# Kernel optimization log

Measured on AMD Instinct MI355X. Metric: run time of the kernel, lower is better.

Reference implementation:

```python
import jax, jax.numpy as jnp
import numpy as np

D_DEC = 256  # decoder_size; W columns are [decoder | encoder] per the torch concat order


def setup_inputs() -> dict:
    key = jax.random.key(0)
    k1, k2, k3, k4 = jax.random.split(key, 4)
    B, S, E, D, A = 32, 4096, 256, 256, 256
    decoder_hidden = jax.random.normal(k1, (1, B, D), dtype=jnp.float32)
    encoder_outputs = jax.random.normal(k2, (S, B, E), dtype=jnp.float32)
    W = jax.random.normal(k3, (A, D + E), dtype=jnp.float32) / np.sqrt(D + E)
    b = jax.random.normal(k4, (A,), dtype=jnp.float32) * 0.02
    return {"decoder_hidden": decoder_hidden, "encoder_outputs": encoder_outputs, "W": W, "b": b}


def reference(decoder_hidden, encoder_outputs, W, b):
    # decoder_hidden: [1,B,D] -> [B,D]; encoder_outputs: [S,B,E] -> [B,S,E]
    dh = decoder_hidden[0]
    eo = jnp.transpose(encoder_outputs, (1, 0, 2))
    # Split the concat-linear: cat([dec, enc]) @ W.T == dec @ Wd.T + enc @ We.T
    Wd, We = W[:, :D_DEC], W[:, D_DEC:]
    # scores: tanh(linear) summed over attn dim -> [B,S]
    proj = dh @ Wd.T + b  # [B,A]
    attn = jnp.tanh(proj[:, None, :] + jnp.einsum('bse,ae->bsa', eo, We))
    scores = jnp.sum(attn, axis=2)  # [B,S]
    attn_softmax = jax.nn.softmax(scores, axis=1)  # [B,S]
    attended = jnp.einsum('bs,bse->be', attn_softmax, eo)  # [B,E]
    encoder_norms = jnp.linalg.norm(eo, axis=2)  # [B,S]
    attn_map = attn_softmax * encoder_norms
    return attended, attn_map
```

## Files before the change

### kernel.cpp

```cpp
#include <hip/hip_runtime.h>
#include <math.h>

#define B_  32
#define S_  4096
#define E_  256
#define A_  256
#define DE_ 512
#define SCH 128

typedef __attribute__((ext_vector_type(8))) short short8;
typedef __attribute__((ext_vector_type(4))) float f32x4;

__device__ inline unsigned short f2bf(float x) {
    unsigned int u = __float_as_uint(x);
    u += 0x7FFFu + ((u >> 16) & 1u);
    return (unsigned short)(u >> 16);
}
__device__ inline float bf2f(unsigned short h) {
    return __uint_as_float(((unsigned int)h) << 16);
}
__device__ inline float tanh_fast(float x) {
    x = fminf(fmaxf(x, -15.f), 15.f);
    float t = __expf(2.f * x);
    return (t - 1.f) * __builtin_amdgcn_rcpf(t + 1.f);
}

__global__ __launch_bounds__(256) void wprep_kernel(
    const float* __restrict__ W, unsigned short* __restrict__ wepk)
{
    const int idx = blockIdx.x * 256 + threadIdx.x;
    const int c     = idx >> 11;
    const int r     = idx & 2047;
    const int plane = r >> 10;
    const int kg    = (r >> 8) & 3;
    const int a     = r & 255;
    const float* src = W + (size_t)a * DE_ + E_ + c * 32 + kg * 8;
    unsigned int pk[4];
    #pragma unroll
    for (int j = 0; j < 4; ++j) {
        float x0 = src[2 * j], x1 = src[2 * j + 1];
        unsigned int u0 = __float_as_uint(x0) & 0xFFFF0000u;
        unsigned int u1 = __float_as_uint(x1) & 0xFFFF0000u;
        if (plane) {
            unsigned short l0 = f2bf(x0 - __uint_as_float(u0));
            unsigned short l1 = f2bf(x1 - __uint_as_float(u1));
            pk[j] = (unsigned int)l0 | ((unsigned int)l1 << 16);
        } else {
            pk[j] = (u0 >> 16) | u1;
        }
    }
    *(uint4*)&wepk[(size_t)idx * 8] = make_uint4(pk[0], pk[1], pk[2], pk[3]);
}

__global__ __launch_bounds__(256) void proj_kernel(
    const float* __restrict__ dh, const float* __restrict__ W,
    const float* __restrict__ bias, float* __restrict__ proj)
{
    __shared__ float dh_lds[E_];
    const int b = blockIdx.x;
    const int a = threadIdx.x;
    dh_lds[a] = dh[b * E_ + a];
    __syncthreads();
    float acc = bias[a];
    const float* wrow = W + (size_t)a * DE_;
    #pragma unroll
    for (int d = 0; d < E_; d += 4) {
        float4 w = *(const float4*)(wrow + d);
        acc += dh_lds[d] * w.x + dh_lds[d+1] * w.y
             + dh_lds[d+2] * w.z + dh_lds[d+3] * w.w;
    }
    proj[b * A_ + a] = acc;
}

__global__ __launch_bounds__(256, 4) void scores_kernel(
    const float* __restrict__ eo,
    const unsigned short* __restrict__ wepk,
    const float* __restrict__ proj,
    float* __restrict__ scores, float* __restrict__ nsq)
{
    __shared__ __align__(16) unsigned short we_hl[2 * 4 * 256 * 8];
    __shared__ __align__(16) unsigned short eo_hl[2 * 4 * 64 * 8];

    const int tid = threadIdx.x;
    const int b   = blockIdx.x & (B_ - 1);
    const int s0  = (blockIdx.x / B_) * 64;
    const int w   = tid >> 6;
    const int l   = tid & 63;
    const int lq  = l >> 4;
    const int lr  = l & 15;
    const int lqx = (lq & 1) << 2;

    float pr[4];
    #pragma unroll
    for (int nt = 0; nt < 4; ++nt) pr[nt] = proj[b * A_ + w * 64 + nt * 16 + lr];

    f32x4 acc[4][4];
    #pragma unroll
    for (int i = 0; i < 4; ++i)
        #pragma unroll
        for (int j = 0; j < 4; ++j)
            acc[i][j] = (f32x4){0.f, 0.f, 0.f, 0.f};

    const int erow0 = tid >> 3;
    const int ekq   = tid & 7;
    const int ekg   = ekq >> 1, ehalf = ekq & 1;
    const int esw   = (ekg & 1) << 2;
    float nacc[2] = {0.f, 0.f};

    for (int kc = 0, c = 0; kc < E_; kc += 32, ++c) {
        __syncthreads();
        #pragma unroll
        for (int it = 0; it < 2; ++it) {
            const int row = it * 32 + erow0;
            float4 v = *(const float4*)(eo + (size_t)(s0 + row) * (B_ * E_)
                                           + b * E_ + kc + ekq * 4);
            nacc[it] += v.x*v.x + v.y*v.y + v.z*v.z + v.w*v.w;
            unsigned int ux = __float_as_uint(v.x) & 0xFFFF0000u;
            unsigned int uy = __float_as_uint(v.y) & 0xFFFF0000u;
            unsigned int uz = __float_as_uint(v.z) & 0xFFFF0000u;
            unsigned int uw = __float_as_uint(v.w) & 0xFFFF0000u;
            unsigned int hp0 = (ux >> 16) | uy;
            unsigned int hp1 = (uz >> 16) | uw;
            unsigned int lp0 = (unsigned int)f2bf(v.x - __uint_as_float(ux))
                             | ((unsigned int)f2bf(v.y - __uint_as_float(uy)) << 16);
            unsigned int lp1 = (unsigned int)f2bf(v.z - __uint_as_float(uz))
                             | ((unsigned int)f2bf(v.w - __uint_as_float(uw)) << 16);
            const int u = ekg * 64 + (row ^ esw);
            *(uint2*)&eo_hl[(size_t)u * 8 + ehalf * 4]         = make_uint2(hp0, hp1);
            *(uint2*)&eo_hl[(size_t)(256 + u) * 8 + ehalf * 4] = make_uint2(lp0, lp1);
        }
        const unsigned short* gsrc = wepk + (size_t)c * 2048 * 8;
        #pragma unroll
        for (int it = 0; it < 8; ++it) {
            const int u = it * 256 + tid;
            __builtin_amdgcn_global_load_lds(
                (const __attribute__((address_space(1))) void*)(gsrc + (size_t)u * 8),
                (__attribute__((address_space(3))) void*)&we_hl[(size_t)u * 8],
                16, 0, 0);
        }
        __syncthreads();
        short8 bh[4], bl[4];
        #pragma unroll
        for (int nt = 0; nt < 4; ++nt) {
            int bunit = lq * 256 + w * 64 + nt * 16 + lr;
            bh[nt] = *(const short8*)&we_hl[(size_t)bunit * 8];
            bl[nt] = *(const short8*)&we_hl[(size_t)(1024 + bunit) * 8];
        }
        #pragma unroll
        for (int mt = 0; mt < 4; ++mt) {
            int aunit = lq * 64 + ((mt * 16 + lr) ^ lqx);
            short8 ah = *(const short8*)&eo_hl[(size_t)aunit * 8];
            short8 al = *(const short8*)&eo_hl[(size_t)(256 + aunit) * 8];
            #pragma unroll
            for (int nt = 0; nt < 4; ++nt) {
                acc[mt][nt] = __builtin_amdgcn_mfma_f32_16x16x32_bf16(ah, bh[nt], acc[mt][nt], 0, 0, 0);
                acc[mt][nt] = __builtin_amdgcn_mfma_f32_16x16x32_bf16(ah, bl[nt], acc[mt][nt], 0, 0, 0);
                acc[mt][nt] = __builtin_amdgcn_mfma_f32_16x16x32_bf16(al, bh[nt], acc[mt][nt], 0, 0, 0);
            }
        }
    }
    __syncthreads();

    float* red4  = (float*)we_hl;
    float* npart = red4 + 64 * 65;
    float* qpart = npart + 512;
    #pragma unroll
    for (int mt = 0; mt < 4; ++mt) {
        #pragma unroll
        for (int r = 0; r < 4; ++r) {
            float s = 0.f;
            #pragma unroll
            for (int nt = 0; nt < 4; ++nt)
                s += tanh_fast(pr[nt] + acc[mt][nt][r]);
            red4[(w * 16 + lr) * 65 + (mt * 16 + lq * 4 + r)] = s;
        }
    }
    npart[tid]       = nacc[0];
    npart[256 + tid] = nacc[1];
    __syncthreads();
    {
        const int r = tid & 63, q = tid >> 6;
        float s = 0.f;
        #pragma unroll
        for (int c2 = q * 16; c2 < q * 16 + 16; ++c2) s += red4[c2 * 65 + r];
        qpart[q * 64 + r] = s;
    }
    __syncthreads();
    if (tid < 64) {
        scores[b * S_ + s0 + tid] = qpart[tid] + qpart[64 + tid]
                                  + qpart[128 + tid] + qpart[192 + tid];
        const int base = (tid >> 5) * 256 + (tid & 31) * 8;
        float nq = 0.f;
        #pragma unroll
        for (int q2 = 0; q2 < 8; ++q2) nq += npart[base + q2];
        nsq[b * S_ + s0 + tid] = nq;
    }
}

__global__ __launch_bounds__(256) void softmax_kernel(
    float* __restrict__ nsq_p, float* __restrict__ out)
{
    __shared__ float red[256];
    const int b = blockIdx.x;
    const int tid = threadIdx.x;
    float* scores = out + B_ * E_;

    float v[16];
    float m = -1e30f;
    #pragma unroll
    for (int i = 0; i < 16; ++i) {
        v[i] = scores[b * S_ + i * 256 + tid];
        m = fmaxf(m, v[i]);
    }
    red[tid] = m;
    __syncthreads();
    for (int off = 128; off > 0; off >>= 1) {
        if (tid < off) red[tid] = fmaxf(red[tid], red[tid + off]);
        __syncthreads();
    }
    m = red[0];
    __syncthreads();
    float sum = 0.f;
    #pragma unroll
    for (int i = 0; i < 16; ++i) { v[i] = expf(v[i] - m); sum += v[i]; }
    red[tid] = sum;
    __syncthreads();
    for (int off = 128; off > 0; off >>= 1) {
        if (tid < off) red[tid] += red[tid + off];
        __syncthreads();
    }
    const float inv = 1.f / red[0];
    #pragma unroll
    for (int i = 0; i < 16; ++i) {
        int s = i * 256 + tid;
        float pp = v[i] * inv;
        float nq = nsq_p[b * S_ + s];
        nsq_p[b * S_ + s] = pp;
        scores[b * S_ + s] = pp * sqrtf(nq);
    }
    out[b * E_ + tid] = 0.f;
}

__global__ __launch_bounds__(256) void attend_kernel(
    const float* __restrict__ eo, const float* __restrict__ p,
    float* __restrict__ out)
{
    __shared__ float4 red[4][64];
    const int tid = threadIdx.x;
    const int b   = blockIdx.x & (B_ - 1);
    const int ch  = blockIdx.x / B_;
    const int le  = tid & 63;
    const int sg  = tid >> 6;
    const int s0  = ch * SCH + sg * (SCH / 4);
    float4 acc = make_float4(0.f, 0.f, 0.f, 0.f);
    #pragma unroll 4
    for (int s = 0; s < SCH / 4; ++s) {
        float pv = p[b * S_ + s0 + s];
        float4 v = *(const float4*)(eo + (size_t)(s0 + s) * (B_ * E_)
                                       + b * E_ + le * 4);
        acc.x = fmaf(pv, v.x, acc.x);
        acc.y = fmaf(pv, v.y, acc.y);
        acc.z = fmaf(pv, v.z, acc.z);
        acc.w = fmaf(pv, v.w, acc.w);
    }
    red[sg][le] = acc;
    __syncthreads();
    if (tid < 64) {
        float4 a0 = red[0][tid], a1 = red[1][tid];
        float4 a2 = red[2][tid], a3 = red[3][tid];
        float* dst = out + b * E_ + tid * 4;
        atomicAdd(dst + 0, a0.x + a1.x + a2.x + a3.x);
        atomicAdd(dst + 1, a0.y + a1.y + a2.y + a3.y);
        atomicAdd(dst + 2, a0.z + a1.z + a2.z + a3.z);
        atomicAdd(dst + 3, a0.w + a1.w + a2.w + a3.w);
    }
}

extern "C" void kernel_launch(void* const* d_in, const int* in_sizes, int n_in,
                              void* d_out, int out_size, void* d_ws, size_t ws_size,
                              hipStream_t stream)
{
    const float* dh   = (const float*)d_in[0];
    const float* eo   = (const float*)d_in[1];
    const float* W    = (const float*)d_in[2];
    const float* bias = (const float*)d_in[3];
    float* out = (float*)d_out;
    float* ws  = (float*)d_ws;

    float* projb = ws;
    float* nsqp  = ws + 8192;
    unsigned short* wepk = (unsigned short*)(ws + 8192 + S_ * B_);
    float* scores = out + B_ * E_;

    wprep_kernel  <<<16384 / 256,     256, 0, stream>>>(W, wepk);
    proj_kernel   <<<B_,              256, 0, stream>>>(dh, W, bias, projb);
    scores_kernel <<<B_ * (S_ / 64),  256, 0, stream>>>(eo, wepk, projb, scores, nsqp);
    softmax_kernel<<<B_,              256, 0, stream>>>(nsqp, out);
    attend_kernel <<<B_ * (S_ / SCH), 256, 0, stream>>>(eo, nsqp, out);
}
```

Baseline: 268.5 us.

## Fuse prep kernels, fold softmax into attend, register-stream W in scores

Merges the W-packing, projection and output-zeroing kernels into one launch. Removes the separate softmax kernel: each attend block recomputes the row max and sum over the scores, then forms probabilities on the fly and writes the attention map. The scores kernel no longer stages W through LDS. It loads W fragments directly into registers, prefetching the next chunk together with the next encoder chunk, and double-buffers the encoder LDS tile so each K step needs one barrier. The costs are redundant softmax reductions in every attend block and higher register pressure, with occupancy lowered to 3 waves.

```diff
diff --git a/kernel.cpp b/kernel.cpp
--- a/kernel.cpp
+++ b/kernel.cpp
@@ -6,7 +6,6 @@
 #define E_  256
 #define A_  256
 #define DE_ 512
-#define SCH 128
 
 typedef __attribute__((ext_vector_type(8))) short short8;
 typedef __attribute__((ext_vector_type(4))) float f32x4;
@@ -16,83 +15,85 @@
     u += 0x7FFFu + ((u >> 16) & 1u);
     return (unsigned short)(u >> 16);
 }
-__device__ inline float bf2f(unsigned short h) {
-    return __uint_as_float(((unsigned int)h) << 16);
-}
 __device__ inline float tanh_fast(float x) {
     x = fminf(fmaxf(x, -15.f), 15.f);
     float t = __expf(2.f * x);
     return (t - 1.f) * __builtin_amdgcn_rcpf(t + 1.f);
 }
 
-__global__ __launch_bounds__(256) void wprep_kernel(
-    const float* __restrict__ W, unsigned short* __restrict__ wepk)
-{
-    const int idx = blockIdx.x * 256 + threadIdx.x;
-    const int c     = idx >> 11;
-    const int r     = idx & 2047;
-    const int plane = r >> 10;
-    const int kg    = (r >> 8) & 3;
-    const int a     = r & 255;
-    const float* src = W + (size_t)a * DE_ + E_ + c * 32 + kg * 8;
-    unsigned int pk[4];
-    #pragma unroll
-    for (int j = 0; j < 4; ++j) {
-        float x0 = src[2 * j], x1 = src[2 * j + 1];
-        unsigned int u0 = __float_as_uint(x0) & 0xFFFF0000u;
-        unsigned int u1 = __float_as_uint(x1) & 0xFFFF0000u;
-        if (plane) {
-            unsigned short l0 = f2bf(x0 - __uint_as_float(u0));
-            unsigned short l1 = f2bf(x1 - __uint_as_float(u1));
-            pk[j] = (unsigned int)l0 | ((unsigned int)l1 << 16);
-        } else {
-            pk[j] = (u0 >> 16) | u1;
-        }
-    }
-    *(uint4*)&wepk[(size_t)idx * 8] = make_uint4(pk[0], pk[1], pk[2], pk[3]);
-}
-
-__global__ __launch_bounds__(256) void proj_kernel(
-    const float* __restrict__ dh, const float* __restrict__ W,
-    const float* __restrict__ bias, float* __restrict__ proj)
+__global__ __launch_bounds__(256) void prep_kernel(
+    const float* __restrict__ W, const float* __restrict__ dh,
+    const float* __restrict__ bias, unsigned short* __restrict__ wepk,
+    float* __restrict__ proj, float* __restrict__ out)
 {
     __shared__ float dh_lds[E_];
-    const int b = blockIdx.x;
-    const int a = threadIdx.x;
-    dh_lds[a] = dh[b * E_ + a];
-    __syncthreads();
-    float acc = bias[a];
-    const float* wrow = W + (size_t)a * DE_;
-    #pragma unroll
-    for (int d = 0; d < E_; d += 4) {
-        float4 w = *(const float4*)(wrow + d);
-        acc += dh_lds[d] * w.x + dh_lds[d+1] * w.y
-             + dh_lds[d+2] * w.z + dh_lds[d+3] * w.w;
-    }
-    proj[b * A_ + a] = acc;
-}
-
-__global__ __launch_bounds__(256, 4) void scores_kernel(
-    const float* __restrict__ eo,
-    const unsigned short* __restrict__ wepk,
+    const int bk  = blockIdx.x;
+    const int tid = threadIdx.x;
+    if (bk < 64) {
+        const int idx = bk * 256 + tid;
+        const int c     = idx >> 11;
+        const int r     = idx & 2047;
+        const int plane = r >> 10;
+        const int kg    = (r >> 8) & 3;
+        const int a     = r & 255;
+        const float* src = W + (size_t)a * DE_ + E_ + c * 32 + kg * 8;
+        unsigned int pk[4];
+        #pragma unroll
+        for (int j = 0; j < 4; ++j) {
+            float x0 = src[2 * j], x1 = src[2 * j + 1];
+            unsigned int u0 = __float_as_uint(x0) & 0xFFFF0000u;
+            unsigned int u1 = __float_as_uint(x1) & 0xFFFF0000u;
+            if (plane) {
+                unsigned short l0 = f2bf(x0 - __uint_as_float(u0));
+                unsigned short l1 = f2bf(x1 - __uint_as_float(u1));
+                pk[j] = (unsigned int)l0 | ((unsigned int)l1 << 16);
+            } else {
+                pk[j] = (u0 >> 16) | u1;
+            }
+        }
+        *(uint4*)&wepk[(size_t)idx * 8] = make_uint4(pk[0], pk[1], pk[2], pk[3]);
+    } else if (bk < 96) {
+        const int b = bk - 64;
+        const int a = tid;
+        dh_lds[a] = dh[b * E_ + a];
+        __syncthreads();
+        float acc = bias[a];
+        const float* wrow = W + (size_t)a * DE_;
+        #pragma unroll
+        for (int d = 0; d < E_; d += 4) {
+            float4 w = *(const float4*)(wrow + d);
+            acc += dh_lds[d] * w.x + dh_lds[d+1] * w.y
+                 + dh_lds[d+2] * w.z + dh_lds[d+3] * w.w;
+        }
+        proj[b * A_ + a] = acc;
+    } else {
+        #pragma unroll
+        for (int j = tid; j < B_ * E_; j += 256) out[j] = 0.f;
+    }
+}
+
+__global__ __launch_bounds__(256, 3) void scores_kernel(
+    const float* __restrict__ eo, const unsigned short* __restrict__ wepk,
     const float* __restrict__ proj,
     float* __restrict__ scores, float* __restrict__ nsq)
 {
-    __shared__ __align__(16) unsigned short we_hl[2 * 4 * 256 * 8];
-    __shared__ __align__(16) unsigned short eo_hl[2 * 4 * 64 * 8];
+    __shared__ __align__(16) unsigned short eo_lds[2 * 528 * 8];
+    __shared__ float red4[64 * 65];
+    __shared__ float npart[512];
+    __shared__ float qpart[256];
 
     const int tid = threadIdx.x;
     const int b   = blockIdx.x & (B_ - 1);
     const int s0  = (blockIdx.x / B_) * 64;
-    const int w   = tid >> 6;
-    const int l   = tid & 63;
-    const int lq  = l >> 4;
-    const int lr  = l & 15;
-    const int lqx = (lq & 1) << 2;
-
-    float pr[4];
-    #pragma unroll
-    for (int nt = 0; nt < 4; ++nt) pr[nt] = proj[b * A_ + w * 64 + nt * 16 + lr];
+    const int w   = tid >> 6, l = tid & 63;
+    const int lq  = l >> 4,  lr = l & 15;
+
+    const int erow0 = tid >> 3;
+    const int ekq   = tid & 7;
+    const int ekg   = ekq >> 1, eh = ekq & 1;
+    const float* ebase = eo + (size_t)(s0 + erow0) * (B_ * E_) + b * E_ + ekq * 4;
+
+    const unsigned short* wb = wepk + (size_t)(lq * 256 + w * 64 + lr) * 8;
 
     f32x4 acc[4][4];
     #pragma unroll
@@ -100,20 +101,23 @@
         #pragma unroll
         for (int j = 0; j < 4; ++j)
             acc[i][j] = (f32x4){0.f, 0.f, 0.f, 0.f};
-
-    const int erow0 = tid >> 3;
-    const int ekq   = tid & 7;
-    const int ekg   = ekq >> 1, ehalf = ekq & 1;
-    const int esw   = (ekg & 1) << 2;
     float nacc[2] = {0.f, 0.f};
 
-    for (int kc = 0, c = 0; kc < E_; kc += 32, ++c) {
-        __syncthreads();
+    float4 ec0 = *(const float4*)(ebase);
+    float4 ec1 = *(const float4*)(ebase + 32 * (B_ * E_));
+    short8 bh[4], bl[4], bnh[4], bnl[4];
+    #pragma unroll
+    for (int nt = 0; nt < 4; ++nt) {
+        bh[nt] = *(const short8*)(wb + (size_t)(nt * 16) * 8);
+        bl[nt] = *(const short8*)(wb + (size_t)(1024 + nt * 16) * 8);
+    }
+
+    #pragma unroll
+    for (int c = 0; c < 8; ++c) {
+        const int wbuf = (c & 1) * 528;
         #pragma unroll
         for (int it = 0; it < 2; ++it) {
-            const int row = it * 32 + erow0;
-            float4 v = *(const float4*)(eo + (size_t)(s0 + row) * (B_ * E_)
-                                           + b * E_ + kc + ekq * 4);
+            float4 v = it ? ec1 : ec0;
             nacc[it] += v.x*v.x + v.y*v.y + v.z*v.z + v.w*v.w;
             unsigned int ux = __float_as_uint(v.x) & 0xFFFF0000u;
             unsigned int uy = __float_as_uint(v.y) & 0xFFFF0000u;
@@ -125,32 +129,25 @@
                              | ((unsigned int)f2bf(v.y - __uint_as_float(uy)) << 16);
             unsigned int lp1 = (unsigned int)f2bf(v.z - __uint_as_float(uz))
                              | ((unsigned int)f2bf(v.w - __uint_as_float(uw)) << 16);
-            const int u = ekg * 64 + (row ^ esw);
-            *(uint2*)&eo_hl[(size_t)u * 8 + ehalf * 4]         = make_uint2(hp0, hp1);
-            *(uint2*)&eo_hl[(size_t)(256 + u) * 8 + ehalf * 4] = make_uint2(lp0, lp1);
-        }
-        const unsigned short* gsrc = wepk + (size_t)c * 2048 * 8;
-        #pragma unroll
-        for (int it = 0; it < 8; ++it) {
-            const int u = it * 256 + tid;
-            __builtin_amdgcn_global_load_lds(
-                (const __attribute__((address_space(1))) void*)(gsrc + (size_t)u * 8),
-                (__attribute__((address_space(3))) void*)&we_hl[(size_t)u * 8],
-                16, 0, 0);
-        }
-        __syncthreads();
-        short8 bh[4], bl[4];
-        #pragma unroll
-        for (int nt = 0; nt < 4; ++nt) {
-            int bunit = lq * 256 + w * 64 + nt * 16 + lr;
-            bh[nt] = *(const short8*)&we_hl[(size_t)bunit * 8];
-            bl[nt] = *(const short8*)&we_hl[(size_t)(1024 + bunit) * 8];
+            const int u = wbuf + ekg * 66 + it * 32 + erow0;
+            *(uint2*)&eo_lds[(size_t)u * 8 + eh * 4]         = make_uint2(hp0, hp1);
+            *(uint2*)&eo_lds[(size_t)(u + 264) * 8 + eh * 4] = make_uint2(lp0, lp1);
+        }
+        __syncthreads();
+        if (c < 7) {
+            ec0 = *(const float4*)(ebase + (c + 1) * 32);
+            ec1 = *(const float4*)(ebase + 32 * (B_ * E_) + (c + 1) * 32);
+            #pragma unroll
+            for (int nt = 0; nt < 4; ++nt) {
+                bnh[nt] = *(const short8*)(wb + (size_t)((c+1)*2048 + nt*16) * 8);
+                bnl[nt] = *(const short8*)(wb + (size_t)((c+1)*2048 + 1024 + nt*16) * 8);
+            }
         }
         #pragma unroll
         for (int mt = 0; mt < 4; ++mt) {
-            int aunit = lq * 64 + ((mt * 16 + lr) ^ lqx);
-            short8 ah = *(const short8*)&eo_hl[(size_t)aunit * 8];
-            short8 al = *(const short8*)&eo_hl[(size_t)(256 + aunit) * 8];
+            const int au = wbuf + lq * 66 + mt * 16 + lr;
+            short8 ah = *(const short8*)&eo_lds[(size_t)au * 8];
+            short8 al = *(const short8*)&eo_lds[(size_t)(au + 264) * 8];
             #pragma unroll
             for (int nt = 0; nt < 4; ++nt) {
                 acc[mt][nt] = __builtin_amdgcn_mfma_f32_16x16x32_bf16(ah, bh[nt], acc[mt][nt], 0, 0, 0);
@@ -158,12 +155,15 @@
                 acc[mt][nt] = __builtin_amdgcn_mfma_f32_16x16x32_bf16(al, bh[nt], acc[mt][nt], 0, 0, 0);
             }
         }
-    }
-    __syncthreads();
-
-    float* red4  = (float*)we_hl;
-    float* npart = red4 + 64 * 65;
-    float* qpart = npart + 512;
+        if (c < 7) {
+            #pragma unroll
+            for (int nt = 0; nt < 4; ++nt) { bh[nt] = bnh[nt]; bl[nt] = bnl[nt]; }
+        }
+    }
+
+    float pr[4];
+    #pragma unroll
+    for (int nt = 0; nt < 4; ++nt) pr[nt] = proj[b * A_ + w * 64 + nt * 16 + lr];
     #pragma unroll
     for (int mt = 0; mt < 4; ++mt) {
         #pragma unroll
@@ -197,13 +197,15 @@
     }
 }
 
-__global__ __launch_bounds__(256) void softmax_kernel(
-    float* __restrict__ nsq_p, float* __restrict__ out)
+__global__ __launch_bounds__(256) void attend_kernel(
+    const float* __restrict__ eo, const float* __restrict__ scores,
+    const float* __restrict__ nsq, float* __restrict__ out)
 {
     __shared__ float red[256];
-    const int b = blockIdx.x;
+    __shared__ float4 acc_red[4][64];
     const int tid = threadIdx.x;
-    float* scores = out + B_ * E_;
+    const int b   = blockIdx.x & (B_ - 1);
+    const int ch  = blockIdx.x / B_;
 
     float v[16];
     float m = -1e30f;
@@ -222,7 +224,7 @@
     __syncthreads();
     float sum = 0.f;
     #pragma unroll
-    for (int i = 0; i < 16; ++i) { v[i] = expf(v[i] - m); sum += v[i]; }
+    for (int i = 0; i < 16; ++i) sum += __expf(v[i] - m);
     red[tid] = sum;
     __syncthreads();
     for (int off = 128; off > 0; off >>= 1) {
@@ -230,44 +232,30 @@
         __syncthreads();
     }
     const float inv = 1.f / red[0];
-    #pragma unroll
-    for (int i = 0; i < 16; ++i) {
-        int s = i * 256 + tid;
-        float pp = v[i] * inv;
-        float nq = nsq_p[b * S_ + s];
-        nsq_p[b * S_ + s] = pp;
-        scores[b * S_ + s] = pp * sqrtf(nq);
-    }
-    out[b * E_ + tid] = 0.f;
-}
-
-__global__ __launch_bounds__(256) void attend_kernel(
-    const float* __restrict__ eo, const float* __restrict__ p,
-    float* __restrict__ out)
-{
-    __shared__ float4 red[4][64];
-    const int tid = threadIdx.x;
-    const int b   = blockIdx.x & (B_ - 1);
-    const int ch  = blockIdx.x / B_;
-    const int le  = tid & 63;
-    const int sg  = tid >> 6;
-    const int s0  = ch * SCH + sg * (SCH / 4);
-    float4 acc = make_float4(0.f, 0.f, 0.f, 0.f);
+
+    const int le = tid & 63, sg = tid >> 6;
+    const int s0 = ch * 128 + sg * 32;
+    float4 a = make_float4(0.f, 0.f, 0.f, 0.f);
     #pragma unroll 4
-    for (int s = 0; s < SCH / 4; ++s) {
-        float pv = p[b * S_ + s0 + s];
-        float4 v = *(const float4*)(eo + (size_t)(s0 + s) * (B_ * E_)
+    for (int s = 0; s < 32; ++s) {
+        float pv = __expf(scores[b * S_ + s0 + s] - m) * inv;
+        float4 e = *(const float4*)(eo + (size_t)(s0 + s) * (B_ * E_)
                                        + b * E_ + le * 4);
-        acc.x = fmaf(pv, v.x, acc.x);
-        acc.y = fmaf(pv, v.y, acc.y);
-        acc.z = fmaf(pv, v.z, acc.z);
-        acc.w = fmaf(pv, v.w, acc.w);
-    }
-    red[sg][le] = acc;
+        a.x = fmaf(pv, e.x, a.x);
+        a.y = fmaf(pv, e.y, a.y);
+        a.z = fmaf(pv, e.z, a.z);
+        a.w = fmaf(pv, e.w, a.w);
+    }
+    acc_red[sg][le] = a;
+    if (tid < 128) {
+        const int s = ch * 128 + tid;
+        float pv = __expf(scores[b * S_ + s] - m) * inv;
+        out[B_ * E_ + b * S_ + s] = pv * sqrtf(nsq[b * S_ + s]);
+    }
     __syncthreads();
     if (tid < 64) {
-        float4 a0 = red[0][tid], a1 = red[1][tid];
-        float4 a2 = red[2][tid], a3 = red[3][tid];
+        float4 a0 = acc_red[0][tid], a1 = acc_red[1][tid];
+        float4 a2 = acc_red[2][tid], a3 = acc_red[3][tid];
         float* dst = out + b * E_ + tid * 4;
         atomicAdd(dst + 0, a0.x + a1.x + a2.x + a3.x);
         atomicAdd(dst + 1, a0.y + a1.y + a2.y + a3.y);
@@ -287,14 +275,12 @@
     float* out = (float*)d_out;
     float* ws  = (float*)d_ws;
 
-    float* projb = ws;
-    float* nsqp  = ws + 8192;
-    unsigned short* wepk = (unsigned short*)(ws + 8192 + S_ * B_);
-    float* scores = out + B_ * E_;
-
-    wprep_kernel  <<<16384 / 256,     256, 0, stream>>>(W, wepk);
-    proj_kernel   <<<B_,              256, 0, stream>>>(dh, W, bias, projb);
-    scores_kernel <<<B_ * (S_ / 64),  256, 0, stream>>>(eo, wepk, projb, scores, nsqp);
-    softmax_kernel<<<B_,              256, 0, stream>>>(nsqp, out);
-    attend_kernel <<<B_ * (S_ / SCH), 256, 0, stream>>>(eo, nsqp, out);
-}
+    float* projb  = ws;
+    float* nsqb   = ws + 8192;
+    float* scores = nsqb + S_ * B_;
+    unsigned short* wepk = (unsigned short*)(scores + S_ * B_);
+
+    prep_kernel   <<<97,              256, 0, stream>>>(W, dh, bias, wepk, projb, out);
+    scores_kernel <<<B_ * (S_ / 64),  256, 0, stream>>>(eo, wepk, projb, scores, nsqb);
+    attend_kernel <<<B_ * (S_ / 128), 256, 0, stream>>>(eo, scores, nsqb, out);
+}
```

New measurement: 273.2 us. About the same (+1.7%).
